# Kernel optimization log

Hardware: AMD Instinct MI355X
Metric: run time of the kernel (lower is better)

## Reference

```python
import jax, jax.numpy as jnp
import numpy as np

B, C, D, H, W = 1, 32, 48, 96, 192


def setup_inputs() -> dict:
    key = jax.random.key(0)
    ks = jax.random.split(key, 5)
    x = jax.random.normal(ks[0], (B, C, D, H, W), dtype=jnp.float32)
    gs = []
    for i in range(4):
        g = jax.random.uniform(ks[i + 1], (B, C, 5, H, W), dtype=jnp.float32)
        # GANet normalizes the 5 aggregation weights to sum to 1 per pixel
        g = g / jnp.sum(g, axis=2, keepdims=True)
        gs.append(g)
    return {"input": x, "g0": gs[0], "g1": gs[1], "g2": gs[2], "g3": gs[3]}


def _sga_dir(cost, g, axis, reverse):
    """Semi-global aggregation along one direction.

    cost: (B,C,D,H,W); g: (B,C,5,H,W). axis=4 scans along width, axis=3 along
    height; reverse flips the scan direction. Recurrence per step p:
      A(p,d) = w0*C(p,d) + w1*A(p-1,d) + w2*A(p-1,d-1) + w3*A(p-1,d+1)
               + w4*max_d' A(p-1,d')
    with A = C at the first position and d+-1 edge-clamped.
    """
    c = jnp.moveaxis(cost, axis, 0)  # (L, B, C, D, R)
    w = jnp.moveaxis(g, axis, 0)     # (L, B, C, 5, R)
    if reverse:
        c = c[::-1]
        w = w[::-1]

    def step(A, xs):
        cs, ws = xs  # cs: (B,C,D,R); ws: (B,C,5,R)
        w0, w1, w2, w3, w4 = (ws[:, :, k][:, :, None] for k in range(5))
        dm1 = jnp.concatenate([A[:, :, :1], A[:, :, :-1]], axis=2)  # d-1 (clamped)
        dp1 = jnp.concatenate([A[:, :, 1:], A[:, :, -1:]], axis=2)  # d+1 (clamped)
        mx = jnp.max(A, axis=2, keepdims=True)                      # max over d
        A_new = w0 * cs + w1 * A + w2 * dm1 + w3 * dp1 + w4 * mx
        return A_new, A_new

    A0 = c[0]
    _, outs = jax.lax.scan(step, A0, (c[1:], w[1:]))
    full = jnp.concatenate([A0[None], outs], axis=0)
    if reverse:
        full = full[::-1]
    return jnp.moveaxis(full, 0, axis)


def reference(input, g0, g1, g2, g3):
    a0 = _sga_dir(input, g0, 4, False)  # left -> right
    a1 = _sga_dir(input, g1, 4, True)   # right -> left
    a2 = _sga_dir(input, g2, 3, False)  # top -> bottom
    a3 = _sga_dir(input, g3, 3, True)   # bottom -> top
    # GANet selects the max over the 4 directions instead of summing
    return jnp.maximum(jnp.maximum(a0, a1), jnp.maximum(a2, a3))
```

## Files before the change

### kernel.cpp

```cpp
#include <hip/hip_runtime.h>

constexpr int Cc = 32;
constexpr int Dd = 48;
constexpr int Hh = 96;
constexpr int Ww = 192;
constexpr int TW = 16;
constexpr int NT = Ww / TW;
constexpr float NEGBIG = -3.402823466e+38f;

template <int CTRL, int RM>
__device__ __forceinline__ float dppmov(float v) {
    int i = __builtin_bit_cast(int, v);
    int r = __builtin_amdgcn_update_dpp(i, i, CTRL, RM, 0xF, false);
    return __builtin_bit_cast(float, r);
}

__device__ __forceinline__ float rdlane(float v, int idx) {
    int r = __builtin_amdgcn_readlane(__builtin_bit_cast(int, v), idx);
    return __builtin_bit_cast(float, r);
}

__device__ __forceinline__ unsigned f2h(float v) {
    return (unsigned)__builtin_bit_cast(unsigned short, (_Float16)v);
}
__device__ __forceinline__ float h2f(unsigned short u) {
    return (float)__builtin_bit_cast(_Float16, u);
}

__device__ __forceinline__ float wave_max48(float v) {
    v = fmaxf(v, dppmov<0x111, 0xF>(v));
    v = fmaxf(v, dppmov<0x112, 0xF>(v));
    v = fmaxf(v, dppmov<0x114, 0xF>(v));
    v = fmaxf(v, dppmov<0x118, 0xF>(v));
    v = fmaxf(v, dppmov<0x142, 0x2>(v));
    v = fmaxf(v, dppmov<0x143, 0x4>(v));
    return rdlane(v, 47);
}

__device__ __forceinline__ float sga_step(float A, float cs, float g0v, float g1v, float g2v,
                                          float g3v, float g4v, bool is47, bool first) {
    float dm1 = dppmov<0x138, 0xF>(A);
    float dp1 = dppmov<0x130, 0xF>(A);
    dp1 = is47 ? A : dp1;
    float mx = wave_max48(A);
    float r = g0v * cs + g1v * A + g2v * dm1 + g3v * dp1 + g4v * mx;
    return first ? cs : r;
}

__global__ __launch_bounds__(64, 4) void sga_w4(const float* __restrict__ x,
                                                const float* __restrict__ ga,
                                                const float* __restrict__ gb,
                                                float* __restrict__ out) {
    __shared__ unsigned sstash[64][Dd];
    __shared__ float xo[Dd][TW + 1];

    const int bid = blockIdx.x;
    const int c = bid / Hh;
    const int h = bid - c * Hh;
    const int lane = threadIdx.x;
    const size_t HW = (size_t)Hh * Ww;

    const float* xrow = x + (size_t)c * Dd * HW + (size_t)h * Ww;
    const float* garow = ga + (size_t)c * 5 * HW + (size_t)h * Ww;
    const float* gbrow = gb + (size_t)c * 5 * HW + (size_t)h * Ww;
    float* orow = out + (size_t)c * Dd * HW + (size_t)h * Ww;

    const int dl = (lane < Dd) ? lane : (Dd - 1);
    const bool is47 = (lane == Dd - 1);

    int srow[3], scol[3];
#pragma unroll
    for (int i = 0; i < 3; ++i) {
        const int e4 = lane + i * 64;
        srow[i] = e4 >> 2;
        scol[i] = (e4 & 3) * 4;
    }
    const int gk = lane >> 4;
    const int gwi = lane & 15;

    float4 pre[3];
    float gA, g4r, gAn = 0.f, g4n = 0.f;
    unsigned tr[8];
    unsigned sv0[8], sv1[8], sv2[8], sv3[8];

    {
#pragma unroll
        for (int i = 0; i < 3; ++i)
            pre[i] = *reinterpret_cast<const float4*>(xrow + (size_t)srow[i] * HW + scol[i]);
        gA = garow[(size_t)gk * HW + gwi];
        g4r = garow[(size_t)4 * HW + gwi];
#pragma unroll
        for (int i = 0; i < 3; ++i) {
            xo[srow[i]][scol[i] + 0] = pre[i].x;
            xo[srow[i]][scol[i] + 1] = pre[i].y;
            xo[srow[i]][scol[i] + 2] = pre[i].z;
            xo[srow[i]][scol[i] + 3] = pre[i].w;
        }
    }

    float A = NEGBIG;

    for (int t = 0; t < NT; ++t) {
        if (t + 1 < NT) {
            const int wn = (t + 1) * TW;
#pragma unroll
            for (int i = 0; i < 3; ++i)
                pre[i] = *reinterpret_cast<const float4*>(xrow + (size_t)srow[i] * HW + wn + scol[i]);
            gAn = garow[(size_t)gk * HW + wn + gwi];
            g4n = garow[(size_t)4 * HW + wn + gwi];
        }
#pragma unroll
        for (int wk = 0; wk < TW; ++wk) {
            const float g0v = rdlane(gA, wk);
            const float g1v = rdlane(gA, 16 + wk);
            const float g2v = rdlane(gA, 32 + wk);
            const float g3v = rdlane(gA, 48 + wk);
            const float g4v = rdlane(g4r, wk);
            const float cs = xo[dl][wk];
            A = sga_step(A, cs, g0v, g1v, g2v, g3v, g4v, is47, (t == 0 && wk == 0));
            const unsigned hu = f2h(A);
            if ((wk & 1) == 0) tr[wk >> 1] = hu;
            else tr[wk >> 1] |= hu << 16;
        }
        if (t < 8) {
            if (lane < Dd) {
#pragma unroll
                for (int r = 0; r < 8; ++r) sstash[t * 8 + r][lane] = tr[r];
            }
        } else if (t == 8) {
#pragma unroll
            for (int r = 0; r < 8; ++r) sv0[r] = tr[r];
        } else if (t == 9) {
#pragma unroll
            for (int r = 0; r < 8; ++r) sv1[r] = tr[r];
        } else if (t == 10) {
#pragma unroll
            for (int r = 0; r < 8; ++r) sv2[r] = tr[r];
        } else {
#pragma unroll
            for (int r = 0; r < 8; ++r) sv3[r] = tr[r];
        }
        if (t + 1 < NT) {
#pragma unroll
            for (int i = 0; i < 3; ++i) {
                xo[srow[i]][scol[i] + 0] = pre[i].x;
                xo[srow[i]][scol[i] + 1] = pre[i].y;
                xo[srow[i]][scol[i] + 2] = pre[i].z;
                xo[srow[i]][scol[i] + 3] = pre[i].w;
            }
            gA = gAn;
            g4r = g4n;
        }
    }

    A = NEGBIG;
    {
        const int w0 = (NT - 1) * TW;
        gA = gbrow[(size_t)gk * HW + w0 + gwi];
        g4r = gbrow[(size_t)4 * HW + w0 + gwi];
    }
    for (int t = NT - 1; t >= 0; --t) {
        const int w0 = t * TW;
        if (t > 0) {
            const int wn = w0 - TW;
#pragma unroll
            for (int i = 0; i < 3; ++i)
                pre[i] = *reinterpret_cast<const float4*>(xrow + (size_t)srow[i] * HW + wn + scol[i]);
            gAn = gbrow[(size_t)gk * HW + wn + gwi];
            g4n = gbrow[(size_t)4 * HW + wn + gwi];
        }
        unsigned rr[8];
        if (t < 8) {
#pragma unroll
            for (int r = 0; r < 8; ++r) rr[r] = sstash[t * 8 + r][dl];
        } else if (t == 8) {
#pragma unroll
            for (int r = 0; r < 8; ++r) rr[r] = sv0[r];
        } else if (t == 9) {
#pragma unroll
            for (int r = 0; r < 8; ++r) rr[r] = sv1[r];
        } else if (t == 10) {
#pragma unroll
            for (int r = 0; r < 8; ++r) rr[r] = sv2[r];
        } else {
#pragma unroll
            for (int r = 0; r < 8; ++r) rr[r] = sv3[r];
        }
#pragma unroll
        for (int wk = TW - 1; wk >= 0; --wk) {
            const float g0v = rdlane(gA, wk);
            const float g1v = rdlane(gA, 16 + wk);
            const float g2v = rdlane(gA, 32 + wk);
            const float g3v = rdlane(gA, 48 + wk);
            const float g4v = rdlane(g4r, wk);
            const float cs = xo[dl][wk];
            A = sga_step(A, cs, g0v, g1v, g2v, g3v, g4v, is47, (t == NT - 1 && wk == TW - 1));
            const unsigned u = rr[wk >> 1];
            const float a0 = h2f((unsigned short)((wk & 1) ? (u >> 16) : (u & 0xffffu)));
            if (lane < Dd) xo[lane][wk] = fmaxf(A, a0);
        }
#pragma unroll
        for (int i = 0; i < 3; ++i) {
            float4 v;
            v.x = xo[srow[i]][scol[i] + 0];
            v.y = xo[srow[i]][scol[i] + 1];
            v.z = xo[srow[i]][scol[i] + 2];
            v.w = xo[srow[i]][scol[i] + 3];
            *reinterpret_cast<float4*>(orow + (size_t)srow[i] * HW + w0 + scol[i]) = v;
        }
        if (t > 0) {
#pragma unroll
            for (int i = 0; i < 3; ++i) {
                xo[srow[i]][scol[i] + 0] = pre[i].x;
                xo[srow[i]][scol[i] + 1] = pre[i].y;
                xo[srow[i]][scol[i] + 2] = pre[i].z;
                xo[srow[i]][scol[i] + 3] = pre[i].w;
            }
            gA = gAn;
            g4r = g4n;
        }
    }
}

constexpr int HWT = 8;
constexpr int HKH = 4;
constexpr int HNP = Hh / HKH;
constexpr int HHALF = HNP / 2;

__global__ __launch_bounds__(1024) void sga_h7(const float* __restrict__ x,
                                               const float* __restrict__ gf,
                                               const float* __restrict__ gr,
                                               float* __restrict__ out) {
    __shared__ _Float16 stash[HWT][2][Hh / 2][Dd];
    __shared__ float xs[2][2][HKH][Dd][9];
    __shared__ float osb[2][2][HKH][Dd][9];
    __shared__ float gs[2][2][HKH][HWT][8];

    const int xcd = blockIdx.x & 7;
    const int within = blockIdx.x >> 3;
    const int pairid = xcd * 48 + (within >> 1);
    const int sub = within & 1;
    const int c = pairid / 12;
    const int w0 = ((pairid % 12) * 2 + sub) * HWT;

    const int tid = threadIdx.x;
    const int lane = tid & 63;
    const int wv = tid >> 6;
    const int col = wv >> 1;
    const int dir = wv & 1;
    const size_t HW = (size_t)Hh * Ww;

    const float* xb = x + (size_t)c * Dd * HW;
    const float* gfb = gf + (size_t)c * 5 * HW;
    const float* grb = gr + (size_t)c * 5 * HW;
    float* ob = out + (size_t)c * Dd * HW;

    const int dl = (lane < Dd) ? lane : (Dd - 1);
    const bool is47 = (lane == Dd - 1);

    int w_[3], d_[3], hp_[3], cu_[3];
    size_t xoff_[3];
#pragma unroll
    for (int j = 0; j < 3; ++j) {
        const int idx = tid + j * 1024;
        w_[j] = idx & 7;
        const int t = idx >> 3;
        d_[j] = t % Dd;
        const int t2 = t / Dd;
        hp_[j] = t2 & 3;
        cu_[j] = t2 >> 2;
        xoff_[j] = (size_t)d_[j] * HW + (w0 + w_[j]);
    }
    const int gw_ = tid & 7;
    const int gk_ = (tid >> 3) % 5;
    const int ghc = (tid >> 3) / 5;
    const int ghp_ = ghc & 3;
    const int gcu_ = ghc >> 2;
    const bool gst = tid < 320;

    auto hofs = [&](int cur, int P, int hp) -> int {
        const int p = P * HKH + hp;
        return cur ? (Hh - 1 - p) : p;
    };

    float xr_[3], grg = 0.f, orr[2][3];

    {
#pragma unroll
        for (int j = 0; j < 3; ++j) xr_[j] = xb[xoff_[j] + (size_t)hofs(cu_[j], 0, hp_[j]) * Ww];
        if (gst) {
            const float* gp = gcu_ ? grb : gfb;
            grg = gp[(size_t)gk_ * HW + (size_t)hofs(gcu_, 0, ghp_) * Ww + (w0 + gw_)];
        }
#pragma unroll
        for (int j = 0; j < 3; ++j) xs[0][cu_[j]][hp_[j]][d_[j]][w_[j]] = xr_[j];
        if (gst) gs[0][gcu_][ghp_][gw_][gk_] = grg;
    }
    __syncthreads();

    float A = NEGBIG;

#pragma unroll 2
    for (int p = 0; p < HNP; ++p) {
        const int pb = p & 1;

        if (p + 1 < HNP) {
#pragma unroll
            for (int j = 0; j < 3; ++j)
                xr_[j] = xb[xoff_[j] + (size_t)hofs(cu_[j], p + 1, hp_[j]) * Ww];
            if (gst) {
                const float* gp = gcu_ ? grb : gfb;
                grg = gp[(size_t)gk_ * HW + (size_t)hofs(gcu_, p + 1, ghp_) * Ww + (w0 + gw_)];
            }
        }
        if (p >= HHALF) {
#pragma unroll
            for (int j = 0; j < 3; ++j)
                orr[pb][j] = ob[xoff_[j] + (size_t)hofs(cu_[j], p, hp_[j]) * Ww];
        }

#pragma unroll
        for (int hp = 0; hp < HKH; ++hp) {
            const int q = p * HKH + hp;
            const float cs = xs[pb][dir][hp][dl][col];
            const float* gbase = &gs[pb][dir][hp][col][0];
            const float4 g03 = *reinterpret_cast<const float4*>(gbase);
            const float g4 = gbase[4];
            A = sga_step(A, cs, g03.x, g03.y, g03.z, g03.w, g4, is47, q == 0);
            if (q < Hh / 2) {
                if (lane < Dd) stash[col][dir][q][lane] = (_Float16)A;
            } else {
                const float s = (float)stash[col][dir ^ 1][Hh - 1 - q][dl];
                const float o = fmaxf(A, s);
                if (lane < Dd) osb[pb][dir][hp][lane][col] = o;
            }
        }

        if (p > HHALF) {
#pragma unroll
            for (int j = 0; j < 3; ++j) {
                const float v = fmaxf(osb[pb ^ 1][cu_[j]][hp_[j]][d_[j]][w_[j]], orr[pb ^ 1][j]);
                ob[xoff_[j] + (size_t)hofs(cu_[j], p - 1, hp_[j]) * Ww] = v;
            }
        }

        if (p + 1 < HNP) {
#pragma unroll
            for (int j = 0; j < 3; ++j) xs[pb ^ 1][cu_[j]][hp_[j]][d_[j]][w_[j]] = xr_[j];
            if (gst) gs[pb ^ 1][gcu_][ghp_][gw_][gk_] = grg;
        }
        __syncthreads();
    }

    {
#pragma unroll
        for (int j = 0; j < 3; ++j) {
            const float v = fmaxf(osb[1][cu_[j]][hp_[j]][d_[j]][w_[j]], orr[1][j]);
            ob[xoff_[j] + (size_t)hofs(cu_[j], HNP - 1, hp_[j]) * Ww] = v;
        }
    }
}

extern "C" void kernel_launch(void* const* d_in, const int* in_sizes, int n_in,
                              void* d_out, int out_size, void* d_ws, size_t ws_size,
                              hipStream_t stream) {
    const float* x  = (const float*)d_in[0];
    const float* g0 = (const float*)d_in[1];
    const float* g1 = (const float*)d_in[2];
    const float* g2 = (const float*)d_in[3];
    const float* g3 = (const float*)d_in[4];
    float* out = (float*)d_out;

    sga_w4<<<Cc * Hh, 64, 0, stream>>>(x, g0, g1, out);
    sga_h7<<<Cc * (Ww / HWT), 1024, 0, stream>>>(x, g2, g3, out);
}
```

Before: 270.7 us.

## Run H-direction scans sequentially per wave with fp16 register stash

Restructures the vertical aggregation kernel so each wave runs the top-to-bottom scan and then the bottom-to-top scan, instead of two waves running them at once. The forward results are packed as fp16 pairs into registers (48 per lane) rather than an LDS stash. This halves the block size to 512 threads, shrinks LDS use and deepens the row tile to 8, so more blocks fit per CU and there are fewer barriers. The cost is that the two directions no longer run in parallel, register pressure rises, and x is read twice.

```diff
diff --git a/kernel.cpp b/kernel.cpp
--- a/kernel.cpp
+++ b/kernel.cpp
@@ -223,18 +223,16 @@
 }
 
 constexpr int HWT = 8;
-constexpr int HKH = 4;
-constexpr int HNP = Hh / HKH;
-constexpr int HHALF = HNP / 2;
-
-__global__ __launch_bounds__(1024) void sga_h7(const float* __restrict__ x,
-                                               const float* __restrict__ gf,
-                                               const float* __restrict__ gr,
-                                               float* __restrict__ out) {
-    __shared__ _Float16 stash[HWT][2][Hh / 2][Dd];
-    __shared__ float xs[2][2][HKH][Dd][9];
-    __shared__ float osb[2][2][HKH][Dd][9];
-    __shared__ float gs[2][2][HKH][HWT][8];
+constexpr int HKH = 8;
+constexpr int HNT = Hh / HKH;
+
+__global__ __launch_bounds__(512, 4) void sga_h8(const float* __restrict__ x,
+                                                 const float* __restrict__ gf,
+                                                 const float* __restrict__ gr,
+                                                 float* __restrict__ out) {
+    __shared__ float xs[2][HKH][Dd][HWT + 1];
+    __shared__ float gs[2][HKH][HWT][8];
+    __shared__ float osb[2][HKH][Dd][HWT + 1];
 
     const int xcd = blockIdx.x & 7;
     const int within = blockIdx.x >> 3;
@@ -245,9 +243,7 @@
 
     const int tid = threadIdx.x;
     const int lane = tid & 63;
-    const int wv = tid >> 6;
-    const int col = wv >> 1;
-    const int dir = wv & 1;
+    const int col = tid >> 6;
     const size_t HW = (size_t)Hh * Ww;
 
     const float* xb = x + (size_t)c * Dd * HW;
@@ -258,105 +254,202 @@
     const int dl = (lane < Dd) ? lane : (Dd - 1);
     const bool is47 = (lane == Dd - 1);
 
-    int w_[3], d_[3], hp_[3], cu_[3];
-    size_t xoff_[3];
-#pragma unroll
-    for (int j = 0; j < 3; ++j) {
-        const int idx = tid + j * 1024;
+    int w_[6], d_[6], hp_[6];
+    size_t xoff_[6];
+#pragma unroll
+    for (int j = 0; j < 6; ++j) {
+        const int idx = tid + j * 512;
         w_[j] = idx & 7;
         const int t = idx >> 3;
         d_[j] = t % Dd;
-        const int t2 = t / Dd;
-        hp_[j] = t2 & 3;
-        cu_[j] = t2 >> 2;
+        hp_[j] = t / Dd;
         xoff_[j] = (size_t)d_[j] * HW + (w0 + w_[j]);
     }
     const int gw_ = tid & 7;
     const int gk_ = (tid >> 3) % 5;
-    const int ghc = (tid >> 3) / 5;
-    const int ghp_ = ghc & 3;
-    const int gcu_ = ghc >> 2;
+    const int ghp_ = (tid >> 3) / 5;
     const bool gst = tid < 320;
 
-    auto hofs = [&](int cur, int P, int hp) -> int {
-        const int p = P * HKH + hp;
-        return cur ? (Hh - 1 - p) : p;
-    };
-
-    float xr_[3], grg = 0.f, orr[2][3];
+    float xr[6], grg = 0.f;
+    unsigned tb[4];
+    unsigned s0[4], s1[4], s2[4], s3[4], s4[4], s5[4];
+    unsigned s6[4], s7[4], s8[4], s9[4], s10[4], s11[4];
 
     {
 #pragma unroll
-        for (int j = 0; j < 3; ++j) xr_[j] = xb[xoff_[j] + (size_t)hofs(cu_[j], 0, hp_[j]) * Ww];
+        for (int j = 0; j < 6; ++j) xr[j] = xb[xoff_[j] + (size_t)hp_[j] * Ww];
+        if (gst) grg = gfb[(size_t)gk_ * HW + (size_t)ghp_ * Ww + (w0 + gw_)];
+#pragma unroll
+        for (int j = 0; j < 6; ++j) xs[0][hp_[j]][d_[j]][w_[j]] = xr[j];
+        if (gst) gs[0][ghp_][gw_][gk_] = grg;
+    }
+    __syncthreads();
+
+    float A = NEGBIG;
+
+#pragma unroll 2
+    for (int t = 0; t < HNT; ++t) {
+        const int pb = t & 1;
+        if (t + 1 < HNT) {
+            const int hb = (t + 1) * HKH;
+#pragma unroll
+            for (int j = 0; j < 6; ++j) xr[j] = xb[xoff_[j] + (size_t)(hb + hp_[j]) * Ww];
+            if (gst) grg = gfb[(size_t)gk_ * HW + (size_t)(hb + ghp_) * Ww + (w0 + gw_)];
+        }
+#pragma unroll
+        for (int hp = 0; hp < HKH; ++hp) {
+            const float cs = xs[pb][hp][dl][col];
+            const float* gb2 = &gs[pb][hp][col][0];
+            const float4 g03 = *reinterpret_cast<const float4*>(gb2);
+            const float g4 = gb2[4];
+            A = sga_step(A, cs, g03.x, g03.y, g03.z, g03.w, g4, is47, (t == 0 && hp == 0));
+            const unsigned hu = f2h(A);
+            if ((hp & 1) == 0) tb[hp >> 1] = hu;
+            else tb[hp >> 1] |= hu << 16;
+        }
+        if (t == 0) {
+#pragma unroll
+            for (int i = 0; i < 4; ++i) s0[i] = tb[i];
+        } else if (t == 1) {
+#pragma unroll
+            for (int i = 0; i < 4; ++i) s1[i] = tb[i];
+        } else if (t == 2) {
+#pragma unroll
+            for (int i = 0; i < 4; ++i) s2[i] = tb[i];
+        } else if (t == 3) {
+#pragma unroll
+            for (int i = 0; i < 4; ++i) s3[i] = tb[i];
+        } else if (t == 4) {
+#pragma unroll
+            for (int i = 0; i < 4; ++i) s4[i] = tb[i];
+        } else if (t == 5) {
+#pragma unroll
+            for (int i = 0; i < 4; ++i) s5[i] = tb[i];
+        } else if (t == 6) {
+#pragma unroll
+            for (int i = 0; i < 4; ++i) s6[i] = tb[i];
+        } else if (t == 7) {
+#pragma unroll
+            for (int i = 0; i < 4; ++i) s7[i] = tb[i];
+        } else if (t == 8) {
+#pragma unroll
+            for (int i = 0; i < 4; ++i) s8[i] = tb[i];
+        } else if (t == 9) {
+#pragma unroll
+            for (int i = 0; i < 4; ++i) s9[i] = tb[i];
+        } else if (t == 10) {
+#pragma unroll
+            for (int i = 0; i < 4; ++i) s10[i] = tb[i];
+        } else {
+#pragma unroll
+            for (int i = 0; i < 4; ++i) s11[i] = tb[i];
+        }
+        if (t + 1 < HNT) {
+#pragma unroll
+            for (int j = 0; j < 6; ++j) xs[pb ^ 1][hp_[j]][d_[j]][w_[j]] = xr[j];
+            if (gst) gs[pb ^ 1][ghp_][gw_][gk_] = grg;
+        }
+        __syncthreads();
+    }
+
+    {
         if (gst) {
-            const float* gp = gcu_ ? grb : gfb;
-            grg = gp[(size_t)gk_ * HW + (size_t)hofs(gcu_, 0, ghp_) * Ww + (w0 + gw_)];
-        }
-#pragma unroll
-        for (int j = 0; j < 3; ++j) xs[0][cu_[j]][hp_[j]][d_[j]][w_[j]] = xr_[j];
-        if (gst) gs[0][gcu_][ghp_][gw_][gk_] = grg;
+            grg = grb[(size_t)gk_ * HW + (size_t)((HNT - 1) * HKH + ghp_) * Ww + (w0 + gw_)];
+            gs[1][ghp_][gw_][gk_] = grg;
+        }
     }
     __syncthreads();
 
-    float A = NEGBIG;
-
+    A = NEGBIG;
+    float orr[2][6];
 #pragma unroll 2
-    for (int p = 0; p < HNP; ++p) {
-        const int pb = p & 1;
-
-        if (p + 1 < HNP) {
-#pragma unroll
-            for (int j = 0; j < 3; ++j)
-                xr_[j] = xb[xoff_[j] + (size_t)hofs(cu_[j], p + 1, hp_[j]) * Ww];
-            if (gst) {
-                const float* gp = gcu_ ? grb : gfb;
-                grg = gp[(size_t)gk_ * HW + (size_t)hofs(gcu_, p + 1, ghp_) * Ww + (w0 + gw_)];
+    for (int r = 0; r < HNT; ++r) {
+        const int t = HNT - 1 - r;
+        const int pb = (r + 1) & 1;
+
+        if (r + 1 < HNT) {
+            const int hb = (t - 1) * HKH;
+#pragma unroll
+            for (int j = 0; j < 6; ++j) xr[j] = xb[xoff_[j] + (size_t)(hb + hp_[j]) * Ww];
+            if (gst) grg = grb[(size_t)gk_ * HW + (size_t)(hb + ghp_) * Ww + (w0 + gw_)];
+        }
+        {
+            const int hb = t * HKH;
+#pragma unroll
+            for (int j = 0; j < 6; ++j)
+                orr[pb][j] = ob[xoff_[j] + (size_t)(hb + hp_[j]) * Ww];
+        }
+        unsigned rb[4];
+        if (t == 0) {
+#pragma unroll
+            for (int i = 0; i < 4; ++i) rb[i] = s0[i];
+        } else if (t == 1) {
+#pragma unroll
+            for (int i = 0; i < 4; ++i) rb[i] = s1[i];
+        } else if (t == 2) {
+#pragma unroll
+            for (int i = 0; i < 4; ++i) rb[i] = s2[i];
+        } else if (t == 3) {
+#pragma unroll
+            for (int i = 0; i < 4; ++i) rb[i] = s3[i];
+        } else if (t == 4) {
+#pragma unroll
+            for (int i = 0; i < 4; ++i) rb[i] = s4[i];
+        } else if (t == 5) {
+#pragma unroll
+            for (int i = 0; i < 4; ++i) rb[i] = s5[i];
+        } else if (t == 6) {
+#pragma unroll
+            for (int i = 0; i < 4; ++i) rb[i] = s6[i];
+        } else if (t == 7) {
+#pragma unroll
+            for (int i = 0; i < 4; ++i) rb[i] = s7[i];
+        } else if (t == 8) {
+#pragma unroll
+            for (int i = 0; i < 4; ++i) rb[i] = s8[i];
+        } else if (t == 9) {
+#pragma unroll
+            for (int i = 0; i < 4; ++i) rb[i] = s9[i];
+        } else if (t == 10) {
+#pragma unroll
+            for (int i = 0; i < 4; ++i) rb[i] = s10[i];
+        } else {
+#pragma unroll
+            for (int i = 0; i < 4; ++i) rb[i] = s11[i];
+        }
+#pragma unroll
+        for (int hp = HKH - 1; hp >= 0; --hp) {
+            const float cs = xs[pb][hp][dl][col];
+            const float* gb2 = &gs[pb][hp][col][0];
+            const float4 g03 = *reinterpret_cast<const float4*>(gb2);
+            const float g4 = gb2[4];
+            A = sga_step(A, cs, g03.x, g03.y, g03.z, g03.w, g4, is47,
+                         (r == 0 && hp == HKH - 1));
+            const unsigned u = rb[hp >> 1];
+            const float a2 = h2f((unsigned short)((hp & 1) ? (u >> 16) : (u & 0xffffu)));
+            if (lane < Dd) osb[pb][hp][lane][col] = fmaxf(A, a2);
+        }
+        if (r > 0) {
+            const int hb = (t + 1) * HKH;
+#pragma unroll
+            for (int j = 0; j < 6; ++j) {
+                const float v = fmaxf(osb[pb ^ 1][hp_[j]][d_[j]][w_[j]], orr[pb ^ 1][j]);
+                ob[xoff_[j] + (size_t)(hb + hp_[j]) * Ww] = v;
             }
         }
-        if (p >= HHALF) {
-#pragma unroll
-            for (int j = 0; j < 3; ++j)
-                orr[pb][j] = ob[xoff_[j] + (size_t)hofs(cu_[j], p, hp_[j]) * Ww];
-        }
-
-#pragma unroll
-        for (int hp = 0; hp < HKH; ++hp) {
-            const int q = p * HKH + hp;
-            const float cs = xs[pb][dir][hp][dl][col];
-            const float* gbase = &gs[pb][dir][hp][col][0];
-            const float4 g03 = *reinterpret_cast<const float4*>(gbase);
-            const float g4 = gbase[4];
-            A = sga_step(A, cs, g03.x, g03.y, g03.z, g03.w, g4, is47, q == 0);
-            if (q < Hh / 2) {
-                if (lane < Dd) stash[col][dir][q][lane] = (_Float16)A;
-            } else {
-                const float s = (float)stash[col][dir ^ 1][Hh - 1 - q][dl];
-                const float o = fmaxf(A, s);
-                if (lane < Dd) osb[pb][dir][hp][lane][col] = o;
-            }
-        }
-
-        if (p > HHALF) {
-#pragma unroll
-            for (int j = 0; j < 3; ++j) {
-                const float v = fmaxf(osb[pb ^ 1][cu_[j]][hp_[j]][d_[j]][w_[j]], orr[pb ^ 1][j]);
-                ob[xoff_[j] + (size_t)hofs(cu_[j], p - 1, hp_[j]) * Ww] = v;
-            }
-        }
-
-        if (p + 1 < HNP) {
-#pragma unroll
-            for (int j = 0; j < 3; ++j) xs[pb ^ 1][cu_[j]][hp_[j]][d_[j]][w_[j]] = xr_[j];
-            if (gst) gs[pb ^ 1][gcu_][ghp_][gw_][gk_] = grg;
+        if (r + 1 < HNT) {
+#pragma unroll
+            for (int j = 0; j < 6; ++j) xs[pb ^ 1][hp_[j]][d_[j]][w_[j]] = xr[j];
+            if (gst) gs[pb ^ 1][ghp_][gw_][gk_] = grg;
         }
         __syncthreads();
     }
 
     {
 #pragma unroll
-        for (int j = 0; j < 3; ++j) {
-            const float v = fmaxf(osb[1][cu_[j]][hp_[j]][d_[j]][w_[j]], orr[1][j]);
-            ob[xoff_[j] + (size_t)hofs(cu_[j], HNP - 1, hp_[j]) * Ww] = v;
+        for (int j = 0; j < 6; ++j) {
+            const float v = fmaxf(osb[0][hp_[j]][d_[j]][w_[j]], orr[0][j]);
+            ob[xoff_[j] + (size_t)hp_[j] * Ww] = v;
         }
     }
 }
@@ -372,5 +465,5 @@
     float* out = (float*)d_out;
 
     sga_w4<<<Cc * Hh, 64, 0, stream>>>(x, g0, g1, out);
-    sga_h7<<<Cc * (Ww / HWT), 1024, 0, stream>>>(x, g2, g3, out);
-}
+    sga_h8<<<Cc * (Ww / HWT), 512, 0, stream>>>(x, g2, g3, out);
+}
```

Result: slower. 436.3 us (+61.1%).

## Process two image rows per wavefront in width-direction SGA kernel

Applied to the files above, without the earlier changes.

The width-direction aggregation kernel now handles two rows (h and h+1) per 64-lane block, interleaving two independent recurrences so their latency-bound DPP/readlane chains overlap. The grid is halved, shared stashes and register save buffers are doubled, launch bounds are relaxed to 2 waves per EU, and the inner loop is unrolled by 8 instead of fully. The trade is more instruction-level parallelism against higher register and LDS pressure, lower occupancy, and fewer blocks.

```diff
diff --git a/kernel.cpp b/kernel.cpp
--- a/kernel.cpp
+++ b/kernel.cpp
@@ -47,23 +47,29 @@
     return first ? cs : r;
 }
 
-__global__ __launch_bounds__(64, 4) void sga_w4(const float* __restrict__ x,
+__global__ __launch_bounds__(64, 2) void sga_w5(const float* __restrict__ x,
                                                 const float* __restrict__ ga,
                                                 const float* __restrict__ gb,
                                                 float* __restrict__ out) {
-    __shared__ unsigned sstash[64][Dd];
-    __shared__ float xo[Dd][TW + 1];
+    __shared__ unsigned sstash0[64][Dd];
+    __shared__ unsigned sstash1[64][Dd];
+    __shared__ float xoA[Dd][TW + 1];
+    __shared__ float xoB[Dd][TW + 1];
 
     const int bid = blockIdx.x;
-    const int c = bid / Hh;
-    const int h = bid - c * Hh;
+    const int c = bid / (Hh / 2);
+    const int h0 = (bid - c * (Hh / 2)) * 2;
     const int lane = threadIdx.x;
     const size_t HW = (size_t)Hh * Ww;
 
-    const float* xrow = x + (size_t)c * Dd * HW + (size_t)h * Ww;
-    const float* garow = ga + (size_t)c * 5 * HW + (size_t)h * Ww;
-    const float* gbrow = gb + (size_t)c * 5 * HW + (size_t)h * Ww;
-    float* orow = out + (size_t)c * Dd * HW + (size_t)h * Ww;
+    const float* xrow0 = x + (size_t)c * Dd * HW + (size_t)h0 * Ww;
+    const float* xrow1 = xrow0 + Ww;
+    const float* garow0 = ga + (size_t)c * 5 * HW + (size_t)h0 * Ww;
+    const float* garow1 = garow0 + Ww;
+    const float* gbrow0 = gb + (size_t)c * 5 * HW + (size_t)h0 * Ww;
+    const float* gbrow1 = gbrow0 + Ww;
+    float* orow0 = out + (size_t)c * Dd * HW + (size_t)h0 * Ww;
+    float* orow1 = orow0 + Ww;
 
     const int dl = (lane < Dd) ? lane : (Dd - 1);
     const bool is47 = (lane == Dd - 1);
@@ -78,146 +84,199 @@
     const int gk = lane >> 4;
     const int gwi = lane & 15;
 
-    float4 pre[3];
-    float gA, g4r, gAn = 0.f, g4n = 0.f;
-    unsigned tr[8];
-    unsigned sv0[8], sv1[8], sv2[8], sv3[8];
+    float4 preA[3], preB[3];
+    float gA0, g40, gA1, g41;
+    float gA0n = 0.f, g40n = 0.f, gA1n = 0.f, g41n = 0.f;
+    unsigned trA[8], trB[8];
+    unsigned a_sv0[8], a_sv1[8], a_sv2[8], a_sv3[8];
+    unsigned b_sv0[8], b_sv1[8], b_sv2[8], b_sv3[8];
 
     {
 #pragma unroll
-        for (int i = 0; i < 3; ++i)
-            pre[i] = *reinterpret_cast<const float4*>(xrow + (size_t)srow[i] * HW + scol[i]);
-        gA = garow[(size_t)gk * HW + gwi];
-        g4r = garow[(size_t)4 * HW + gwi];
-#pragma unroll
         for (int i = 0; i < 3; ++i) {
-            xo[srow[i]][scol[i] + 0] = pre[i].x;
-            xo[srow[i]][scol[i] + 1] = pre[i].y;
-            xo[srow[i]][scol[i] + 2] = pre[i].z;
-            xo[srow[i]][scol[i] + 3] = pre[i].w;
-        }
-    }
-
-    float A = NEGBIG;
+            preA[i] = *reinterpret_cast<const float4*>(xrow0 + (size_t)srow[i] * HW + scol[i]);
+            preB[i] = *reinterpret_cast<const float4*>(xrow1 + (size_t)srow[i] * HW + scol[i]);
+        }
+        gA0 = garow0[(size_t)gk * HW + gwi];
+        g40 = garow0[(size_t)4 * HW + gwi];
+        gA1 = garow1[(size_t)gk * HW + gwi];
+        g41 = garow1[(size_t)4 * HW + gwi];
+#pragma unroll
+        for (int i = 0; i < 3; ++i) {
+            xoA[srow[i]][scol[i] + 0] = preA[i].x;
+            xoA[srow[i]][scol[i] + 1] = preA[i].y;
+            xoA[srow[i]][scol[i] + 2] = preA[i].z;
+            xoA[srow[i]][scol[i] + 3] = preA[i].w;
+            xoB[srow[i]][scol[i] + 0] = preB[i].x;
+            xoB[srow[i]][scol[i] + 1] = preB[i].y;
+            xoB[srow[i]][scol[i] + 2] = preB[i].z;
+            xoB[srow[i]][scol[i] + 3] = preB[i].w;
+        }
+    }
+
+    float A0 = NEGBIG, A1 = NEGBIG;
 
     for (int t = 0; t < NT; ++t) {
         if (t + 1 < NT) {
             const int wn = (t + 1) * TW;
 #pragma unroll
-            for (int i = 0; i < 3; ++i)
-                pre[i] = *reinterpret_cast<const float4*>(xrow + (size_t)srow[i] * HW + wn + scol[i]);
-            gAn = garow[(size_t)gk * HW + wn + gwi];
-            g4n = garow[(size_t)4 * HW + wn + gwi];
-        }
-#pragma unroll
+            for (int i = 0; i < 3; ++i) {
+                preA[i] = *reinterpret_cast<const float4*>(xrow0 + (size_t)srow[i] * HW + wn + scol[i]);
+                preB[i] = *reinterpret_cast<const float4*>(xrow1 + (size_t)srow[i] * HW + wn + scol[i]);
+            }
+            gA0n = garow0[(size_t)gk * HW + wn + gwi];
+            g40n = garow0[(size_t)4 * HW + wn + gwi];
+            gA1n = garow1[(size_t)gk * HW + wn + gwi];
+            g41n = garow1[(size_t)4 * HW + wn + gwi];
+        }
+#pragma unroll 8
         for (int wk = 0; wk < TW; ++wk) {
-            const float g0v = rdlane(gA, wk);
-            const float g1v = rdlane(gA, 16 + wk);
-            const float g2v = rdlane(gA, 32 + wk);
-            const float g3v = rdlane(gA, 48 + wk);
-            const float g4v = rdlane(g4r, wk);
-            const float cs = xo[dl][wk];
-            A = sga_step(A, cs, g0v, g1v, g2v, g3v, g4v, is47, (t == 0 && wk == 0));
-            const unsigned hu = f2h(A);
-            if ((wk & 1) == 0) tr[wk >> 1] = hu;
-            else tr[wk >> 1] |= hu << 16;
+            const bool first = (t == 0 && wk == 0);
+            const float csA = xoA[dl][wk];
+            const float csB = xoB[dl][wk];
+            A0 = sga_step(A0, csA, rdlane(gA0, wk), rdlane(gA0, 16 + wk),
+                          rdlane(gA0, 32 + wk), rdlane(gA0, 48 + wk), rdlane(g40, wk),
+                          is47, first);
+            A1 = sga_step(A1, csB, rdlane(gA1, wk), rdlane(gA1, 16 + wk),
+                          rdlane(gA1, 32 + wk), rdlane(gA1, 48 + wk), rdlane(g41, wk),
+                          is47, first);
+            const unsigned huA = f2h(A0);
+            const unsigned huB = f2h(A1);
+            if ((wk & 1) == 0) {
+                trA[wk >> 1] = huA;
+                trB[wk >> 1] = huB;
+            } else {
+                trA[wk >> 1] |= huA << 16;
+                trB[wk >> 1] |= huB << 16;
+            }
         }
         if (t < 8) {
             if (lane < Dd) {
 #pragma unroll
-                for (int r = 0; r < 8; ++r) sstash[t * 8 + r][lane] = tr[r];
+                for (int r = 0; r < 8; ++r) {
+                    sstash0[t * 8 + r][lane] = trA[r];
+                    sstash1[t * 8 + r][lane] = trB[r];
+                }
             }
         } else if (t == 8) {
 #pragma unroll
-            for (int r = 0; r < 8; ++r) sv0[r] = tr[r];
+            for (int r = 0; r < 8; ++r) { a_sv0[r] = trA[r]; b_sv0[r] = trB[r]; }
         } else if (t == 9) {
 #pragma unroll
-            for (int r = 0; r < 8; ++r) sv1[r] = tr[r];
+            for (int r = 0; r < 8; ++r) { a_sv1[r] = trA[r]; b_sv1[r] = trB[r]; }
         } else if (t == 10) {
 #pragma unroll
-            for (int r = 0; r < 8; ++r) sv2[r] = tr[r];
+            for (int r = 0; r < 8; ++r) { a_sv2[r] = trA[r]; b_sv2[r] = trB[r]; }
         } else {
 #pragma unroll
-            for (int r = 0; r < 8; ++r) sv3[r] = tr[r];
+            for (int r = 0; r < 8; ++r) { a_sv3[r] = trA[r]; b_sv3[r] = trB[r]; }
         }
         if (t + 1 < NT) {
 #pragma unroll
             for (int i = 0; i < 3; ++i) {
-                xo[srow[i]][scol[i] + 0] = pre[i].x;
-                xo[srow[i]][scol[i] + 1] = pre[i].y;
-                xo[srow[i]][scol[i] + 2] = pre[i].z;
-                xo[srow[i]][scol[i] + 3] = pre[i].w;
-            }
-            gA = gAn;
-            g4r = g4n;
-        }
-    }
-
-    A = NEGBIG;
+                xoA[srow[i]][scol[i] + 0] = preA[i].x;
+                xoA[srow[i]][scol[i] + 1] = preA[i].y;
+                xoA[srow[i]][scol[i] + 2] = preA[i].z;
+                xoA[srow[i]][scol[i] + 3] = preA[i].w;
+                xoB[srow[i]][scol[i] + 0] = preB[i].x;
+                xoB[srow[i]][scol[i] + 1] = preB[i].y;
+                xoB[srow[i]][scol[i] + 2] = preB[i].z;
+                xoB[srow[i]][scol[i] + 3] = preB[i].w;
+            }
+            gA0 = gA0n; g40 = g40n; gA1 = gA1n; g41 = g41n;
+        }
+    }
+
+    A0 = NEGBIG;
+    A1 = NEGBIG;
     {
         const int w0 = (NT - 1) * TW;
-        gA = gbrow[(size_t)gk * HW + w0 + gwi];
-        g4r = gbrow[(size_t)4 * HW + w0 + gwi];
+        gA0 = gbrow0[(size_t)gk * HW + w0 + gwi];
+        g40 = gbrow0[(size_t)4 * HW + w0 + gwi];
+        gA1 = gbrow1[(size_t)gk * HW + w0 + gwi];
+        g41 = gbrow1[(size_t)4 * HW + w0 + gwi];
     }
     for (int t = NT - 1; t >= 0; --t) {
         const int w0 = t * TW;
         if (t > 0) {
             const int wn = w0 - TW;
 #pragma unroll
-            for (int i = 0; i < 3; ++i)
-                pre[i] = *reinterpret_cast<const float4*>(xrow + (size_t)srow[i] * HW + wn + scol[i]);
-            gAn = gbrow[(size_t)gk * HW + wn + gwi];
-            g4n = gbrow[(size_t)4 * HW + wn + gwi];
-        }
-        unsigned rr[8];
+            for (int i = 0; i < 3; ++i) {
+                preA[i] = *reinterpret_cast<const float4*>(xrow0 + (size_t)srow[i] * HW + wn + scol[i]);
+                preB[i] = *reinterpret_cast<const float4*>(xrow1 + (size_t)srow[i] * HW + wn + scol[i]);
+            }
+            gA0n = gbrow0[(size_t)gk * HW + wn + gwi];
+            g40n = gbrow0[(size_t)4 * HW + wn + gwi];
+            gA1n = gbrow1[(size_t)gk * HW + wn + gwi];
+            g41n = gbrow1[(size_t)4 * HW + wn + gwi];
+        }
+        unsigned rrA[8], rrB[8];
         if (t < 8) {
 #pragma unroll
-            for (int r = 0; r < 8; ++r) rr[r] = sstash[t * 8 + r][dl];
+            for (int r = 0; r < 8; ++r) {
+                rrA[r] = sstash0[t * 8 + r][dl];
+                rrB[r] = sstash1[t * 8 + r][dl];
+            }
         } else if (t == 8) {
 #pragma unroll
-            for (int r = 0; r < 8; ++r) rr[r] = sv0[r];
+            for (int r = 0; r < 8; ++r) { rrA[r] = a_sv0[r]; rrB[r] = b_sv0[r]; }
         } else if (t == 9) {
 #pragma unroll
-            for (int r = 0; r < 8; ++r) rr[r] = sv1[r];
+            for (int r = 0; r < 8; ++r) { rrA[r] = a_sv1[r]; rrB[r] = b_sv1[r]; }
         } else if (t == 10) {
 #pragma unroll
-            for (int r = 0; r < 8; ++r) rr[r] = sv2[r];
+            for (int r = 0; r < 8; ++r) { rrA[r] = a_sv2[r]; rrB[r] = b_sv2[r]; }
         } else {
 #pragma unroll
-            for (int r = 0; r < 8; ++r) rr[r] = sv3[r];
-        }
-#pragma unroll
+            for (int r = 0; r < 8; ++r) { rrA[r] = a_sv3[r]; rrB[r] = b_sv3[r]; }
+        }
+#pragma unroll 8
         for (int wk = TW - 1; wk >= 0; --wk) {
-            const float g0v = rdlane(gA, wk);
-            const float g1v = rdlane(gA, 16 + wk);
-            const float g2v = rdlane(gA, 32 + wk);
-            const float g3v = rdlane(gA, 48 + wk);
-            const float g4v = rdlane(g4r, wk);
-            const float cs = xo[dl][wk];
-            A = sga_step(A, cs, g0v, g1v, g2v, g3v, g4v, is47, (t == NT - 1 && wk == TW - 1));
-            const unsigned u = rr[wk >> 1];
-            const float a0 = h2f((unsigned short)((wk & 1) ? (u >> 16) : (u & 0xffffu)));
-            if (lane < Dd) xo[lane][wk] = fmaxf(A, a0);
+            const bool first = (t == NT - 1 && wk == TW - 1);
+            const float csA = xoA[dl][wk];
+            const float csB = xoB[dl][wk];
+            A0 = sga_step(A0, csA, rdlane(gA0, wk), rdlane(gA0, 16 + wk),
+                          rdlane(gA0, 32 + wk), rdlane(gA0, 48 + wk), rdlane(g40, wk),
+                          is47, first);
+            A1 = sga_step(A1, csB, rdlane(gA1, wk), rdlane(gA1, 16 + wk),
+                          rdlane(gA1, 32 + wk), rdlane(gA1, 48 + wk), rdlane(g41, wk),
+                          is47, first);
+            const unsigned uA = rrA[wk >> 1];
+            const unsigned uB = rrB[wk >> 1];
+            const float a0A = h2f((unsigned short)((wk & 1) ? (uA >> 16) : (uA & 0xffffu)));
+            const float a0B = h2f((unsigned short)((wk & 1) ? (uB >> 16) : (uB & 0xffffu)));
+            if (lane < Dd) {
+                xoA[lane][wk] = fmaxf(A0, a0A);
+                xoB[lane][wk] = fmaxf(A1, a0B);
+            }
         }
 #pragma unroll
         for (int i = 0; i < 3; ++i) {
-            float4 v;
-            v.x = xo[srow[i]][scol[i] + 0];
-            v.y = xo[srow[i]][scol[i] + 1];
-            v.z = xo[srow[i]][scol[i] + 2];
-            v.w = xo[srow[i]][scol[i] + 3];
-            *reinterpret_cast<float4*>(orow + (size_t)srow[i] * HW + w0 + scol[i]) = v;
+            float4 v0, v1;
+            v0.x = xoA[srow[i]][scol[i] + 0];
+            v0.y = xoA[srow[i]][scol[i] + 1];
+            v0.z = xoA[srow[i]][scol[i] + 2];
+            v0.w = xoA[srow[i]][scol[i] + 3];
+            v1.x = xoB[srow[i]][scol[i] + 0];
+            v1.y = xoB[srow[i]][scol[i] + 1];
+            v1.z = xoB[srow[i]][scol[i] + 2];
+            v1.w = xoB[srow[i]][scol[i] + 3];
+            *reinterpret_cast<float4*>(orow0 + (size_t)srow[i] * HW + w0 + scol[i]) = v0;
+            *reinterpret_cast<float4*>(orow1 + (size_t)srow[i] * HW + w0 + scol[i]) = v1;
         }
         if (t > 0) {
 #pragma unroll
             for (int i = 0; i < 3; ++i) {
-                xo[srow[i]][scol[i] + 0] = pre[i].x;
-                xo[srow[i]][scol[i] + 1] = pre[i].y;
-                xo[srow[i]][scol[i] + 2] = pre[i].z;
-                xo[srow[i]][scol[i] + 3] = pre[i].w;
-            }
-            gA = gAn;
-            g4r = g4n;
+                xoA[srow[i]][scol[i] + 0] = preA[i].x;
+                xoA[srow[i]][scol[i] + 1] = preA[i].y;
+                xoA[srow[i]][scol[i] + 2] = preA[i].z;
+                xoA[srow[i]][scol[i] + 3] = preA[i].w;
+                xoB[srow[i]][scol[i] + 0] = preB[i].x;
+                xoB[srow[i]][scol[i] + 1] = preB[i].y;
+                xoB[srow[i]][scol[i] + 2] = preB[i].z;
+                xoB[srow[i]][scol[i] + 3] = preB[i].w;
+            }
+            gA0 = gA0n; g40 = g40n; gA1 = gA1n; g41 = g41n;
         }
     }
 }
@@ -371,6 +430,6 @@
     const float* g3 = (const float*)d_in[4];
     float* out = (float*)d_out;
 
-    sga_w4<<<Cc * Hh, 64, 0, stream>>>(x, g0, g1, out);
+    sga_w5<<<Cc * (Hh / 2), 64, 0, stream>>>(x, g0, g1, out);
     sga_h7<<<Cc * (Ww / HWT), 1024, 0, stream>>>(x, g2, g3, out);
 }
```

New measurement: 404.2 us. +49.3%, slower.

## Run forward and backward width scans concurrently in two waves per block

Applied to the files above, without the earlier changes.

The width-direction kernel now uses two wavefronts per block, one for the left-to-right scan and one for the right-to-left scan, instead of running them one after the other in a single wave. Each wave stashes its first half of results in half precision in shared memory. After a barrier at the midpoint, each wave reads the other's stash, combines with max and writes the output for its second half. This halves the serial dependency chain per row. It costs a block-wide barrier and more shared memory per block, and register stash arrays are dropped.

```diff
diff --git a/kernel.cpp b/kernel.cpp
--- a/kernel.cpp
+++ b/kernel.cpp
@@ -47,22 +47,54 @@
     return first ? cs : r;
 }
 
-__global__ __launch_bounds__(64, 4) void sga_w4(const float* __restrict__ x,
-                                                const float* __restrict__ ga,
-                                                const float* __restrict__ gb,
-                                                float* __restrict__ out) {
-    __shared__ unsigned sstash[64][Dd];
-    __shared__ float xo[Dd][TW + 1];
+template <bool DESC, bool STASH>
+__device__ __forceinline__ void w6_run16(float& A, unsigned* tr, const unsigned* rr,
+                                         float (*xo)[TW + 1], float gA, float g4r,
+                                         int lane, int dl, bool is47, bool firstTile) {
+#pragma unroll
+    for (int k = 0; k < TW; ++k) {
+        const int wk = DESC ? (TW - 1 - k) : k;
+        const float g0v = rdlane(gA, wk);
+        const float g1v = rdlane(gA, 16 + wk);
+        const float g2v = rdlane(gA, 32 + wk);
+        const float g3v = rdlane(gA, 48 + wk);
+        const float g4v = rdlane(g4r, wk);
+        const float cs = xo[dl][wk];
+        A = sga_step(A, cs, g0v, g1v, g2v, g3v, g4v, is47, firstTile && (k == 0));
+        if (STASH) {
+            const unsigned hu = f2h(A);
+            if (!DESC) {
+                if ((wk & 1) == 0) tr[wk >> 1] = hu;
+                else tr[wk >> 1] |= hu << 16;
+            } else {
+                if (wk & 1) tr[wk >> 1] = hu << 16;
+                else tr[wk >> 1] |= hu;
+            }
+        } else {
+            const unsigned u = rr[wk >> 1];
+            const float aop = h2f((unsigned short)((wk & 1) ? (u >> 16) : (u & 0xffffu)));
+            if (lane < Dd) xo[lane][wk] = fmaxf(A, aop);
+        }
+    }
+}
+
+__global__ __launch_bounds__(128, 4) void sga_w6(const float* __restrict__ x,
+                                                 const float* __restrict__ ga,
+                                                 const float* __restrict__ gb,
+                                                 float* __restrict__ out) {
+    __shared__ unsigned sstash[2][48][Dd];
+    __shared__ float xo[2][Dd][TW + 1];
 
     const int bid = blockIdx.x;
     const int c = bid / Hh;
     const int h = bid - c * Hh;
-    const int lane = threadIdx.x;
+    const int tid = threadIdx.x;
+    const int lane = tid & 63;
+    const int dir = tid >> 6;
     const size_t HW = (size_t)Hh * Ww;
 
     const float* xrow = x + (size_t)c * Dd * HW + (size_t)h * Ww;
-    const float* garow = ga + (size_t)c * 5 * HW + (size_t)h * Ww;
-    const float* gbrow = gb + (size_t)c * 5 * HW + (size_t)h * Ww;
+    const float* grow = (dir ? gb : ga) + (size_t)c * 5 * HW + (size_t)h * Ww;
     float* orow = out + (size_t)c * Dd * HW + (size_t)h * Ww;
 
     const int dl = (lane < Dd) ? lane : (Dd - 1);
@@ -81,140 +113,79 @@
     float4 pre[3];
     float gA, g4r, gAn = 0.f, g4n = 0.f;
     unsigned tr[8];
-    unsigned sv0[8], sv1[8], sv2[8], sv3[8];
 
     {
+        const int t = dir ? (NT - 1) : 0;
+        const int w0 = t * TW;
 #pragma unroll
         for (int i = 0; i < 3; ++i)
-            pre[i] = *reinterpret_cast<const float4*>(xrow + (size_t)srow[i] * HW + scol[i]);
-        gA = garow[(size_t)gk * HW + gwi];
-        g4r = garow[(size_t)4 * HW + gwi];
+            pre[i] = *reinterpret_cast<const float4*>(xrow + (size_t)srow[i] * HW + w0 + scol[i]);
+        gA = grow[(size_t)gk * HW + w0 + gwi];
+        g4r = grow[(size_t)4 * HW + w0 + gwi];
 #pragma unroll
         for (int i = 0; i < 3; ++i) {
-            xo[srow[i]][scol[i] + 0] = pre[i].x;
-            xo[srow[i]][scol[i] + 1] = pre[i].y;
-            xo[srow[i]][scol[i] + 2] = pre[i].z;
-            xo[srow[i]][scol[i] + 3] = pre[i].w;
+            xo[dir][srow[i]][scol[i] + 0] = pre[i].x;
+            xo[dir][srow[i]][scol[i] + 1] = pre[i].y;
+            xo[dir][srow[i]][scol[i] + 2] = pre[i].z;
+            xo[dir][srow[i]][scol[i] + 3] = pre[i].w;
         }
     }
 
     float A = NEGBIG;
 
-    for (int t = 0; t < NT; ++t) {
-        if (t + 1 < NT) {
-            const int wn = (t + 1) * TW;
+    for (int tt = 0; tt < NT; ++tt) {
+        if (tt == NT / 2) __syncthreads();
+
+        const int t = dir ? (NT - 1 - tt) : tt;
+        const int w0 = t * TW;
+
+        if (tt + 1 < NT) {
+            const int wn = (dir ? (NT - 2 - tt) : (tt + 1)) * TW;
 #pragma unroll
             for (int i = 0; i < 3; ++i)
                 pre[i] = *reinterpret_cast<const float4*>(xrow + (size_t)srow[i] * HW + wn + scol[i]);
-            gAn = garow[(size_t)gk * HW + wn + gwi];
-            g4n = garow[(size_t)4 * HW + wn + gwi];
-        }
-#pragma unroll
-        for (int wk = 0; wk < TW; ++wk) {
-            const float g0v = rdlane(gA, wk);
-            const float g1v = rdlane(gA, 16 + wk);
-            const float g2v = rdlane(gA, 32 + wk);
-            const float g3v = rdlane(gA, 48 + wk);
-            const float g4v = rdlane(g4r, wk);
-            const float cs = xo[dl][wk];
-            A = sga_step(A, cs, g0v, g1v, g2v, g3v, g4v, is47, (t == 0 && wk == 0));
-            const unsigned hu = f2h(A);
-            if ((wk & 1) == 0) tr[wk >> 1] = hu;
-            else tr[wk >> 1] |= hu << 16;
-        }
-        if (t < 8) {
+            gAn = grow[(size_t)gk * HW + wn + gwi];
+            g4n = grow[(size_t)4 * HW + wn + gwi];
+        }
+
+        unsigned rr[8];
+        if (tt >= NT / 2) {
+#pragma unroll
+            for (int r = 0; r < 8; ++r) rr[r] = sstash[dir ^ 1][(NT - 1 - tt) * 8 + r][dl];
+        }
+
+        if (tt < NT / 2) {
+            if (dir == 0)
+                w6_run16<false, true>(A, tr, rr, xo[0], gA, g4r, lane, dl, is47, tt == 0);
+            else
+                w6_run16<true, true>(A, tr, rr, xo[1], gA, g4r, lane, dl, is47, tt == 0);
             if (lane < Dd) {
 #pragma unroll
-                for (int r = 0; r < 8; ++r) sstash[t * 8 + r][lane] = tr[r];
-            }
-        } else if (t == 8) {
-#pragma unroll
-            for (int r = 0; r < 8; ++r) sv0[r] = tr[r];
-        } else if (t == 9) {
-#pragma unroll
-            for (int r = 0; r < 8; ++r) sv1[r] = tr[r];
-        } else if (t == 10) {
-#pragma unroll
-            for (int r = 0; r < 8; ++r) sv2[r] = tr[r];
+                for (int r = 0; r < 8; ++r) sstash[dir][tt * 8 + r][lane] = tr[r];
+            }
         } else {
-#pragma unroll
-            for (int r = 0; r < 8; ++r) sv3[r] = tr[r];
-        }
-        if (t + 1 < NT) {
+            if (dir == 0)
+                w6_run16<false, false>(A, tr, rr, xo[0], gA, g4r, lane, dl, is47, false);
+            else
+                w6_run16<true, false>(A, tr, rr, xo[1], gA, g4r, lane, dl, is47, false);
 #pragma unroll
             for (int i = 0; i < 3; ++i) {
-                xo[srow[i]][scol[i] + 0] = pre[i].x;
-                xo[srow[i]][scol[i] + 1] = pre[i].y;
-                xo[srow[i]][scol[i] + 2] = pre[i].z;
-                xo[srow[i]][scol[i] + 3] = pre[i].w;
-            }
-            gA = gAn;
-            g4r = g4n;
-        }
-    }
-
-    A = NEGBIG;
-    {
-        const int w0 = (NT - 1) * TW;
-        gA = gbrow[(size_t)gk * HW + w0 + gwi];
-        g4r = gbrow[(size_t)4 * HW + w0 + gwi];
-    }
-    for (int t = NT - 1; t >= 0; --t) {
-        const int w0 = t * TW;
-        if (t > 0) {
-            const int wn = w0 - TW;
-#pragma unroll
-            for (int i = 0; i < 3; ++i)
-                pre[i] = *reinterpret_cast<const float4*>(xrow + (size_t)srow[i] * HW + wn + scol[i]);
-            gAn = gbrow[(size_t)gk * HW + wn + gwi];
-            g4n = gbrow[(size_t)4 * HW + wn + gwi];
-        }
-        unsigned rr[8];
-        if (t < 8) {
-#pragma unroll
-            for (int r = 0; r < 8; ++r) rr[r] = sstash[t * 8 + r][dl];
-        } else if (t == 8) {
-#pragma unroll
-            for (int r = 0; r < 8; ++r) rr[r] = sv0[r];
-        } else if (t == 9) {
-#pragma unroll
-            for (int r = 0; r < 8; ++r) rr[r] = sv1[r];
-        } else if (t == 10) {
-#pragma unroll
-            for (int r = 0; r < 8; ++r) rr[r] = sv2[r];
-        } else {
-#pragma unroll
-            for (int r = 0; r < 8; ++r) rr[r] = sv3[r];
-        }
-#pragma unroll
-        for (int wk = TW - 1; wk >= 0; --wk) {
-            const float g0v = rdlane(gA, wk);
-            const float g1v = rdlane(gA, 16 + wk);
-            const float g2v = rdlane(gA, 32 + wk);
-            const float g3v = rdlane(gA, 48 + wk);
-            const float g4v = rdlane(g4r, wk);
-            const float cs = xo[dl][wk];
-            A = sga_step(A, cs, g0v, g1v, g2v, g3v, g4v, is47, (t == NT - 1 && wk == TW - 1));
-            const unsigned u = rr[wk >> 1];
-            const float a0 = h2f((unsigned short)((wk & 1) ? (u >> 16) : (u & 0xffffu)));
-            if (lane < Dd) xo[lane][wk] = fmaxf(A, a0);
-        }
-#pragma unroll
-        for (int i = 0; i < 3; ++i) {
-            float4 v;
-            v.x = xo[srow[i]][scol[i] + 0];
-            v.y = xo[srow[i]][scol[i] + 1];
-            v.z = xo[srow[i]][scol[i] + 2];
-            v.w = xo[srow[i]][scol[i] + 3];
-            *reinterpret_cast<float4*>(orow + (size_t)srow[i] * HW + w0 + scol[i]) = v;
-        }
-        if (t > 0) {
+                float4 v;
+                v.x = xo[dir][srow[i]][scol[i] + 0];
+                v.y = xo[dir][srow[i]][scol[i] + 1];
+                v.z = xo[dir][srow[i]][scol[i] + 2];
+                v.w = xo[dir][srow[i]][scol[i] + 3];
+                *reinterpret_cast<float4*>(orow + (size_t)srow[i] * HW + w0 + scol[i]) = v;
+            }
+        }
+
+        if (tt + 1 < NT) {
 #pragma unroll
             for (int i = 0; i < 3; ++i) {
-                xo[srow[i]][scol[i] + 0] = pre[i].x;
-                xo[srow[i]][scol[i] + 1] = pre[i].y;
-                xo[srow[i]][scol[i] + 2] = pre[i].z;
-                xo[srow[i]][scol[i] + 3] = pre[i].w;
+                xo[dir][srow[i]][scol[i] + 0] = pre[i].x;
+                xo[dir][srow[i]][scol[i] + 1] = pre[i].y;
+                xo[dir][srow[i]][scol[i] + 2] = pre[i].z;
+                xo[dir][srow[i]][scol[i] + 3] = pre[i].w;
             }
             gA = gAn;
             g4r = g4n;
@@ -371,6 +342,6 @@
     const float* g3 = (const float*)d_in[4];
     float* out = (float*)d_out;
 
-    sga_w4<<<Cc * Hh, 64, 0, stream>>>(x, g0, g1, out);
+    sga_w6<<<Cc * Hh, 128, 0, stream>>>(x, g0, g1, out);
     sga_h7<<<Cc * (Ww / HWT), 1024, 0, stream>>>(x, g2, g3, out);
 }
```

Result: faster. 250.4 us (-7.5%).
